# Performance work log

Hardware: AMD Instinct MI355X
Metric: run time of the kernel (lower is better)

Reference implementation:

```python
import jax, jax.numpy as jnp
import numpy as np

N = 100000   # nodes
E = 1600000  # edges
D = 128      # d_model
FF = 512     # dim_feedforward
EPS = 1e-5


def setup_inputs() -> dict:
    key = jax.random.key(0)
    ks = jax.random.split(key, 12)
    x = jax.random.normal(ks[0], (N, D), dtype=jnp.float32)
    edge_index = jax.random.randint(ks[1], (2, E), 0, N, dtype=jnp.int64)
    edge_weight = jax.random.uniform(ks[2], (E,), dtype=jnp.float32)
    sD = 1.0 / np.sqrt(D)
    sFF = 1.0 / np.sqrt(FF)
    W = jax.random.normal(ks[3], (D, D), dtype=jnp.float32) * sD   # GCN weight
    b = jnp.zeros((D,), jnp.float32)                                # GCN bias
    gamma = jnp.ones((D,), jnp.float32)                             # shared batchnorm
    beta = jnp.zeros((D,), jnp.float32)
    W1 = jax.random.normal(ks[4], (D, FF), dtype=jnp.float32) * sD  # MLP lin1
    b1 = jnp.zeros((FF,), jnp.float32)
    W2 = jax.random.normal(ks[5], (FF, D), dtype=jnp.float32) * sFF # MLP lin2
    b2 = jnp.zeros((D,), jnp.float32)
    return {"x": x, "edge_index": edge_index, "edge_weight": edge_weight,
            "W": W, "b": b, "gamma": gamma, "beta": beta,
            "W1": W1, "b1": b1, "W2": W2, "b2": b2}


def gcn_conv(x, edge_index, edge_weight, W, b):
    # GCNConv with add_self_loops=True (self-loop weight 1) and symmetric norm.
    h = x @ W                                   # [N, D]
    src, dst = edge_index[0], edge_index[1]
    deg = jax.ops.segment_sum(edge_weight, dst, num_segments=N) + 1.0
    dinv = jnp.where(deg > 0, jax.lax.rsqrt(deg), 0.0)
    norm = dinv[src] * edge_weight * dinv[dst]  # [E]
    out = jax.ops.segment_sum(norm[:, None] * h[src], dst, num_segments=N)
    out = out + (dinv * dinv)[:, None] * h      # self-loop contribution
    return out + b


def batch_norm(x, gamma, beta):
    # training-mode BatchNorm1d over the node (batch) dimension
    mu = jnp.mean(x, axis=0)
    var = jnp.mean((x - mu) ** 2, axis=0)
    return gamma * (x - mu) * jax.lax.rsqrt(var + EPS) + beta


def reference(x, edge_index, edge_weight, W, b, gamma, beta, W1, b1, W2, b2):
    x1 = batch_norm(x + gcn_conv(x, edge_index, edge_weight, W, b), gamma, beta)
    x2 = jax.nn.relu(x1 @ W1 + b1) @ W2 + b2    # MLP d_model->dim_ff->d_model
    return batch_norm(x1 + x2, gamma, beta)
```

## Files before the change

kernel.cpp:

```cpp
#include <hip/hip_runtime.h>

#define NN 100000
#define EE 1600000
#define DD 128
#define FFD 512
#define EPSV 1e-5f

#define SCB 98
#define EB 6250
#define MIXB 18750

typedef __attribute__((ext_vector_type(8))) short bf16x8;
typedef __attribute__((ext_vector_type(4))) float f32x4;
typedef unsigned long long ull;

__device__ __forceinline__ ushort f2b(float f) {
    uint u = __float_as_uint(f);
    return (ushort)((u + 0x7FFF + ((u >> 16) & 1)) >> 16);
}
__device__ __forceinline__ float b2f(ushort u) {
    return __uint_as_float(((uint)u) << 16);
}

__device__ __forceinline__ void gld_lds16(const ushort* g, ushort* l) {
    __builtin_amdgcn_global_load_lds(
        (const __attribute__((address_space(1))) uint*)g,
        (__attribute__((address_space(3))) uint*)l, 16, 0, 0);
}


__global__ __launch_bounds__(256) void k_init(ull* pk, float* s1, float* s2) {
    int i = blockIdx.x * 256 + threadIdx.x;
    if (i < NN) pk[i] = 0ULL;
    if (blockIdx.x == 0) { s1[threadIdx.x] = 0.f; s2[threadIdx.x] = 0.f; }
}


__global__ __launch_bounds__(256) void k_pre(const int* __restrict__ ei,
                                             const float* __restrict__ ew,
                                             ull* __restrict__ pk,
                                             int* __restrict__ rank,
                                             const float* __restrict__ x,
                                             ushort* __restrict__ xb,
                                             const float* __restrict__ W,
                                             const float* __restrict__ W1,
                                             const float* __restrict__ W2,
                                             ushort* __restrict__ WTb,
                                             ushort* __restrict__ W1img,
                                             ushort* __restrict__ W2img) {
    int bid = blockIdx.x;
    int t = threadIdx.x;
    if (bid < MIXB) {
        if (bid % 3 == 0) {
            int e = (bid / 3) * 256 + t;
            int dst = ei[EE + e];
            uint fx = (uint)(ew[e] * 16777216.0f + 0.5f);
            ull old = atomicAdd(&pk[dst], (1ULL << 32) | (ull)fx);
            rank[e] = (int)(old >> 32);
        } else {
            int xbk = bid - bid / 3 - 1;
            long i = (long)xbk * 256 + t;
            float4 v = ((const float4*)x)[i];
            ushort4 o;
            o.x = f2b(v.x); o.y = f2b(v.y); o.z = f2b(v.z); o.w = f2b(v.w);
            ((ushort4*)xb)[i] = o;
        }
    } else {
        int i = (bid - MIXB) * 256 + t;
        if (i < 16384) {
            int n = i >> 7, k = i & 127;
            WTb[i] = f2b(W[k * 128 + n]);
        } else if (i < 16384 + 65536) {
            int u = i - 16384;
            int ch = u >> 14, rem = u & 16383;
            int f = rem >> 7, col = rem & 127;
            int kb = (col >> 3) ^ (f & 15);
            int j = col & 7;
            W1img[u] = f2b(W1[(kb * 8 + j) * 512 + ch * 128 + f]);
        } else {
            int u = i - 16384 - 65536;
            int ch = u >> 14, rem = u & 16383;
            int jrow = rem >> 7, col = rem & 127;
            int kb = (col >> 3) ^ (jrow & 15);
            int j2 = col & 7;
            W2img[u] = f2b(W2[(ch * 128 + kb * 8 + j2) * 128 + jrow]);
        }
    }
}


__global__ __launch_bounds__(256) void k_scan_part(const ull* __restrict__ pk,
                                                   int* __restrict__ cnt,
                                                   float* __restrict__ dinv,
                                                   int* __restrict__ bsum) {
    __shared__ int red[4];
    int b = blockIdx.x, t = threadIdx.x;
    int base = b * 1024 + t * 4;
    int s = 0;
#pragma unroll
    for (int j = 0; j < 4; ++j) {
        int i = base + j;
        if (i < NN) {
            ull v = pk[i];
            int c = (int)(v >> 32);
            cnt[i] = c;
            dinv[i] = rsqrtf(1.0f + (float)(uint)(v & 0xFFFFFFFFu) * (1.0f / 16777216.0f));
            s += c;
        }
    }
#pragma unroll
    for (int d = 1; d < 64; d <<= 1) s += __shfl_xor(s, d);
    if ((t & 63) == 0) red[t >> 6] = s;
    __syncthreads();
    if (t == 0) bsum[b] = red[0] + red[1] + red[2] + red[3];
}

__global__ __launch_bounds__(128) void k_scan_base(int* __restrict__ bsum,
                                                   int* __restrict__ bbase,
                                                   int* __restrict__ start) {
    if (threadIdx.x == 0) {
        int run = 0;
        for (int i = 0; i < SCB; ++i) { bbase[i] = run; run += bsum[i]; }
        start[NN] = run;
    }
}

__global__ __launch_bounds__(256) void k_scan_fin(const int* __restrict__ cnt,
                                                  const int* __restrict__ bbase,
                                                  int* __restrict__ start) {
    __shared__ int ts[256];
    int b = blockIdx.x, t = threadIdx.x;
    int base = b * 1024 + t * 4;
    int v[4];
    int s = 0;
#pragma unroll
    for (int j = 0; j < 4; ++j) {
        int i = base + j;
        v[j] = (i < NN) ? cnt[i] : 0;
        s += v[j];
    }
    ts[t] = s;
    __syncthreads();
    for (int d = 1; d < 256; d <<= 1) {
        int add = (t >= d) ? ts[t - d] : 0;
        __syncthreads();
        ts[t] += add;
        __syncthreads();
    }
    int run = bbase[b] + ts[t] - s;
#pragma unroll
    for (int j = 0; j < 4; ++j) {
        int i = base + j;
        if (i < NN) {
            start[i] = run;
            run += v[j];
        }
    }
}


__global__ __launch_bounds__(256) void k_fill(const int* __restrict__ ei,
                                              const float* __restrict__ ew,
                                              const float* __restrict__ dinv,
                                              const int* __restrict__ start,
                                              const int* __restrict__ rank,
                                              uint2* __restrict__ csr) {
    int e = blockIdx.x * 256 + threadIdx.x;
    if (e < EE) {
        int src = ei[e];
        int dst = ei[EE + e];
        float nrm = dinv[src] * ew[e] * dinv[dst];
        int pos = start[dst] + rank[e];
        csr[pos] = make_uint2((uint)src, __float_as_uint(nrm));
    }
}


__global__ __launch_bounds__(256) void k_gather(const ushort* __restrict__ xb,
                                                const float* __restrict__ dinv,
                                                const int* __restrict__ start,
                                                const uint2* __restrict__ csr,
                                                ushort* __restrict__ aggx) {
    int t = threadIdx.x;
    int wv = t >> 6, l = t & 63;
    const uint* xbu = (const uint*)xb;
    uint* aggu = (uint*)aggx;

    for (int k = 0; k < 8; ++k) {
        int node = blockIdx.x * 32 + wv * 8 + k;
        int e0 = start[node], e1 = start[node + 1];
        float a0 = 0.f, a1 = 0.f;
        int i = e0;
        for (; i + 8 <= e1; i += 8) {
            uint2 rr[8];
            uint hh[8];
#pragma unroll
            for (int u = 0; u < 8; ++u) rr[u] = csr[i + u];
#pragma unroll
            for (int u = 0; u < 8; ++u) hh[u] = xbu[rr[u].x * 64 + l];
#pragma unroll
            for (int u = 0; u < 8; ++u) {
                float n = __uint_as_float(rr[u].y);
                a0 = fmaf(n, b2f((ushort)(hh[u] & 0xFFFF)), a0);
                a1 = fmaf(n, b2f((ushort)(hh[u] >> 16)), a1);
            }
        }
        if (i + 4 <= e1) {
            uint2 rr[4];
            uint hh[4];
#pragma unroll
            for (int u = 0; u < 4; ++u) rr[u] = csr[i + u];
#pragma unroll
            for (int u = 0; u < 4; ++u) hh[u] = xbu[rr[u].x * 64 + l];
#pragma unroll
            for (int u = 0; u < 4; ++u) {
                float n = __uint_as_float(rr[u].y);
                a0 = fmaf(n, b2f((ushort)(hh[u] & 0xFFFF)), a0);
                a1 = fmaf(n, b2f((ushort)(hh[u] >> 16)), a1);
            }
            i += 4;
        }
        for (; i < e1; ++i) {
            uint2 r0 = csr[i];
            uint h0 = xbu[r0.x * 64 + l];
            float n0 = __uint_as_float(r0.y);
            a0 = fmaf(n0, b2f((ushort)(h0 & 0xFFFF)), a0);
            a1 = fmaf(n0, b2f((ushort)(h0 >> 16)), a1);
        }
        float dv = dinv[node];
        float sl = dv * dv;
        uint hs = xbu[node * 64 + l];
        a0 = fmaf(sl, b2f((ushort)(hs & 0xFFFF)), a0);
        a1 = fmaf(sl, b2f((ushort)(hs >> 16)), a1);
        aggu[node * 64 + l] = (uint)f2b(a0) | ((uint)f2b(a1) << 16);
    }
}


__global__ __launch_bounds__(256) void k_conv(const ushort* __restrict__ aggx,
                                              const ushort* __restrict__ WTb,
                                              const float* __restrict__ b,
                                              ushort* xyb,
                                              float* __restrict__ stats1) {
    __shared__ __align__(16) ushort xt[64][136];
    __shared__ __align__(16) ushort wt[128][136];
    int t = threadIdx.x;
    int row0 = blockIdx.x * 64;

    for (int i = t; i < 2048; i += 256) {
        int r = i >> 4, c8 = (i & 15) << 3;
        *(uint4*)&wt[r][c8] = ((const uint4*)WTb)[i];
    }
    for (int i = t; i < 1024; i += 256) {
        int r = i >> 4, c8 = (i & 15) << 3;
        int gr = row0 + r;
        uint4 v = make_uint4(0u, 0u, 0u, 0u);
        if (gr < NN) v = ((const uint4*)aggx)[(long)gr * 16 + (i & 15)];
        *(uint4*)&xt[r][c8] = v;
    }
    __syncthreads();

    int wv = t >> 6, l = t & 63;
    int lr = l & 15, lg = l >> 4;
    int rw = wv & 1, jw = wv >> 1;

    f32x4 z4 = {0.f, 0.f, 0.f, 0.f};
    f32x4 acc[4][2];
#pragma unroll
    for (int jt = 0; jt < 4; ++jt)
#pragma unroll
        for (int rt = 0; rt < 2; ++rt) acc[jt][rt] = z4;

#pragma unroll
    for (int ks = 0; ks < 4; ++ks) {
        bf16x8 qR0 = *(const bf16x8*)&xt[rw * 32 + lr][ks * 32 + lg * 8];
        bf16x8 qR1 = *(const bf16x8*)&xt[rw * 32 + 16 + lr][ks * 32 + lg * 8];
#pragma unroll
        for (int jt = 0; jt < 4; ++jt) {
            bf16x8 pW = *(const bf16x8*)&wt[jw * 64 + jt * 16 + lr][ks * 32 + lg * 8];
            acc[jt][0] = __builtin_amdgcn_mfma_f32_16x16x32_bf16(pW, qR0, acc[jt][0], 0, 0, 0);
            acc[jt][1] = __builtin_amdgcn_mfma_f32_16x16x32_bf16(pW, qR1, acc[jt][1], 0, 0, 0);
        }
    }

    float sj[4][4], qj[4][4];
#pragma unroll
    for (int jt = 0; jt < 4; ++jt)
#pragma unroll
        for (int g = 0; g < 4; ++g) { sj[jt][g] = 0.f; qj[jt][g] = 0.f; }

#pragma unroll
    for (int jt = 0; jt < 4; ++jt) {
        int jb = jw * 64 + jt * 16 + lg * 4;
        float4 bv = *(const float4*)&b[jb];
#pragma unroll
        for (int rt = 0; rt < 2; ++rt) {
            int rloc = rw * 32 + rt * 16 + lr;
            int r = row0 + rloc;
            if (r < NN) {
                ushort4 xv = *(const ushort4*)&xyb[(long)r * 128 + jb];
                float z0 = b2f(xv.x) + acc[jt][rt][0] + bv.x;
                float z1 = b2f(xv.y) + acc[jt][rt][1] + bv.y;
                float z2 = b2f(xv.z) + acc[jt][rt][2] + bv.z;
                float z3 = b2f(xv.w) + acc[jt][rt][3] + bv.w;
                ushort4 o;
                o.x = f2b(z0); o.y = f2b(z1); o.z = f2b(z2); o.w = f2b(z3);
                *(ushort4*)&xyb[(long)r * 128 + jb] = o;
                sj[jt][0] += z0; sj[jt][1] += z1; sj[jt][2] += z2; sj[jt][3] += z3;
                qj[jt][0] += z0 * z0; qj[jt][1] += z1 * z1; qj[jt][2] += z2 * z2; qj[jt][3] += z3 * z3;
            }
        }
    }
#pragma unroll
    for (int jt = 0; jt < 4; ++jt)
#pragma unroll
        for (int g = 0; g < 4; ++g) {
#pragma unroll
            for (int d = 1; d < 16; d <<= 1) {
                sj[jt][g] += __shfl_xor(sj[jt][g], d);
                qj[jt][g] += __shfl_xor(qj[jt][g], d);
            }
        }
    __syncthreads();
    float* redS = (float*)&xt[0][0];
    float* redQ = redS + 512;
    if (lr == 0) {
#pragma unroll
        for (int jt = 0; jt < 4; ++jt)
#pragma unroll
            for (int g = 0; g < 4; ++g) {
                int j = jw * 64 + jt * 16 + lg * 4 + g;
                redS[wv * 128 + j] = sj[jt][g];
                redQ[wv * 128 + j] = qj[jt][g];
            }
    }
    __syncthreads();
    if (t < 128) {
        int w0 = (t >> 6) * 2;
        atomicAdd(&stats1[t], redS[w0 * 128 + t] + redS[(w0 + 1) * 128 + t]);
        atomicAdd(&stats1[128 + t], redQ[w0 * 128 + t] + redQ[(w0 + 1) * 128 + t]);
    }
}


__global__ __launch_bounds__(128) void k_bn_fin(const float* __restrict__ stats,
                                                const float* __restrict__ gamma,
                                                const float* __restrict__ beta,
                                                float* __restrict__ ac) {
    int c = threadIdx.x;
    float mu = stats[c] * (1.0f / NN);
    float var = stats[128 + c] * (1.0f / NN) - mu * mu;
    float a = gamma[c] * rsqrtf(var + EPSV);
    ac[c] = a;
    ac[128 + c] = beta[c] - mu * a;
}


__global__ __launch_bounds__(256) void k_affine2(const ushort* __restrict__ zb,
                                                 const float* __restrict__ ac,
                                                 float* __restrict__ out) {
    long i = (long)blockIdx.x * 256 + threadIdx.x;
    int c4i = (int)(i & 31);
    float4 a = ((const float4*)ac)[c4i];
    float4 cc = ((const float4*)(ac + 128))[c4i];
    ushort4 zv = ((const ushort4*)zb)[i];
    float4 o;
    o.x = a.x * b2f(zv.x) + cc.x;
    o.y = a.y * b2f(zv.y) + cc.y;
    o.z = a.z * b2f(zv.z) + cc.z;
    o.w = a.w * b2f(zv.w) + cc.w;
    ((float4*)out)[i] = o;
}


#define SWZ16(row, kb) ((((kb) ^ ((row) & 15)) << 3))

__global__ __launch_bounds__(512, 4) void k_mlp(const ushort* __restrict__ yb,
                                                const float* __restrict__ ac1,
                                                const ushort* __restrict__ W1img,
                                                const float* __restrict__ b1,
                                                const ushort* __restrict__ W2img,
                                                const float* __restrict__ b2,
                                                ushort* __restrict__ zb,
                                                float* __restrict__ stats2) {
    __shared__ __align__(16) ushort xt[64 * 128];
    __shared__ __align__(16) ushort ht[64 * 128];
    __shared__ __align__(16) ushort wc[128 * 128];
    int t = threadIdx.x;
    int row0 = blockIdx.x * 64;

    for (int i = t; i < 1024; i += 512) {
        int r = i >> 4, kb = i & 15;
        int gr = row0 + r;
        ushort4 y0 = make_ushort4(0, 0, 0, 0), y1 = make_ushort4(0, 0, 0, 0);
        if (gr < NN) {
            long base = (long)gr * 32 + kb * 2;
            y0 = ((const ushort4*)yb)[base];
            y1 = ((const ushort4*)yb)[base + 1];
        }
        float4 a0 = ((const float4*)ac1)[kb * 2];
        float4 a1 = ((const float4*)ac1)[kb * 2 + 1];
        float4 c0 = ((const float4*)(ac1 + 128))[kb * 2];
        float4 c1 = ((const float4*)(ac1 + 128))[kb * 2 + 1];
        ushort4 o0, o1;
        o0.x = f2b(a0.x * b2f(y0.x) + c0.x);
        o0.y = f2b(a0.y * b2f(y0.y) + c0.y);
        o0.z = f2b(a0.z * b2f(y0.z) + c0.z);
        o0.w = f2b(a0.w * b2f(y0.w) + c0.w);
        o1.x = f2b(a1.x * b2f(y1.x) + c1.x);
        o1.y = f2b(a1.y * b2f(y1.y) + c1.y);
        o1.z = f2b(a1.z * b2f(y1.z) + c1.z);
        o1.w = f2b(a1.w * b2f(y1.w) + c1.w);
        ushort* dst = &xt[r * 128 + SWZ16(r, kb)];
        *(ushort4*)dst = o0;
        *(ushort4*)(dst + 4) = o1;
    }

    int wv = t >> 6, l = t & 63;
    int lr = l & 15, lg = l >> 4;
    int rw = wv & 3, jw = wv >> 2;
    int xrow = rw * 16 + lr;

    f32x4 z4 = {0.f, 0.f, 0.f, 0.f};
    f32x4 acc[4];
#pragma unroll
    for (int jt = 0; jt < 4; ++jt) acc[jt] = z4;

    for (int ch = 0; ch < 4; ++ch) {
        __syncthreads();
        {
            const ushort* src = W1img + ch * 16384;
#pragma unroll
            for (int i = 0; i < 4; ++i) {
                int u = (t + i * 512) * 8;
                gld_lds16(src + u, wc + u);
            }
        }
        __syncthreads();

        f32x4 hacc[4];
#pragma unroll
        for (int ft = 0; ft < 4; ++ft) hacc[ft] = z4;
#pragma unroll
        for (int ks = 0; ks < 4; ++ks) {
            int kcol = ((ks * 4 + lg) ^ lr) << 3;
            bf16x8 aR = *(const bf16x8*)&xt[xrow * 128 + kcol];
#pragma unroll
            for (int ft = 0; ft < 4; ++ft) {
                int f = jw * 64 + ft * 16 + lr;
                bf16x8 bW = *(const bf16x8*)&wc[f * 128 + kcol];
                hacc[ft] = __builtin_amdgcn_mfma_f32_16x16x32_bf16(aR, bW, hacc[ft], 0, 0, 0);
            }
        }
#pragma unroll
        for (int ft = 0; ft < 4; ++ft) {
            int fcol = jw * 64 + ft * 16 + lr;
            float b1v = b1[ch * 128 + fcol];
            int kbf = fcol >> 3, wi = fcol & 7;
#pragma unroll
            for (int rg = 0; rg < 4; ++rg) {
                int hrow = rw * 16 + lg * 4 + rg;
                ht[hrow * 128 + ((kbf ^ (hrow & 15)) << 3) + wi] =
                    f2b(fmaxf(hacc[ft][rg] + b1v, 0.f));
            }
        }
        __syncthreads();

        {
            const ushort* src = W2img + ch * 16384;
#pragma unroll
            for (int i = 0; i < 4; ++i) {
                int u = (t + i * 512) * 8;
                gld_lds16(src + u, wc + u);
            }
        }
        __syncthreads();

#pragma unroll
        for (int ks = 0; ks < 4; ++ks) {
            int kcol = ((ks * 4 + lg) ^ lr) << 3;
            bf16x8 qR = *(const bf16x8*)&ht[xrow * 128 + kcol];
#pragma unroll
            for (int jt = 0; jt < 4; ++jt) {
                int j = jw * 64 + jt * 16 + lr;
                bf16x8 pW = *(const bf16x8*)&wc[j * 128 + kcol];
                acc[jt] = __builtin_amdgcn_mfma_f32_16x16x32_bf16(pW, qR, acc[jt], 0, 0, 0);
            }
        }
    }

    float sj[4][4], qj[4][4];
    int r = row0 + xrow;
#pragma unroll
    for (int jt = 0; jt < 4; ++jt) {
        int jb = jw * 64 + jt * 16 + lg * 4;
        float4 b2v = *(const float4*)&b2[jb];
        int kbj = jb >> 3, wj = jb & 7;
        ushort4 xv = *(const ushort4*)&xt[xrow * 128 + ((kbj ^ lr) << 3) + wj];
        float z0 = b2f(xv.x) + acc[jt][0] + b2v.x;
        float z1 = b2f(xv.y) + acc[jt][1] + b2v.y;
        float z2 = b2f(xv.z) + acc[jt][2] + b2v.z;
        float z3 = b2f(xv.w) + acc[jt][3] + b2v.w;
        if (r < NN) {
            ushort4 o;
            o.x = f2b(z0); o.y = f2b(z1); o.z = f2b(z2); o.w = f2b(z3);
            *(ushort4*)&zb[(long)r * 128 + jb] = o;
            sj[jt][0] = z0; sj[jt][1] = z1; sj[jt][2] = z2; sj[jt][3] = z3;
            qj[jt][0] = z0 * z0; qj[jt][1] = z1 * z1; qj[jt][2] = z2 * z2; qj[jt][3] = z3 * z3;
        } else {
            sj[jt][0] = 0.f; sj[jt][1] = 0.f; sj[jt][2] = 0.f; sj[jt][3] = 0.f;
            qj[jt][0] = 0.f; qj[jt][1] = 0.f; qj[jt][2] = 0.f; qj[jt][3] = 0.f;
        }
    }
#pragma unroll
    for (int jt = 0; jt < 4; ++jt)
#pragma unroll
        for (int g = 0; g < 4; ++g) {
#pragma unroll
            for (int d = 1; d < 16; d <<= 1) {
                sj[jt][g] += __shfl_xor(sj[jt][g], d);
                qj[jt][g] += __shfl_xor(qj[jt][g], d);
            }
        }
    __syncthreads();
    float* redS = (float*)&ht[0];
    float* redQ = redS + 1024;
    if (lr == 0) {
#pragma unroll
        for (int jt = 0; jt < 4; ++jt)
#pragma unroll
            for (int g = 0; g < 4; ++g) {
                int j = jw * 64 + jt * 16 + lg * 4 + g;
                redS[wv * 128 + j] = sj[jt][g];
                redQ[wv * 128 + j] = qj[jt][g];
            }
    }
    __syncthreads();
    if (t < 128) {
        int h = t >> 6;
        float S = redS[(h * 4 + 0) * 128 + t] + redS[(h * 4 + 1) * 128 + t]
                + redS[(h * 4 + 2) * 128 + t] + redS[(h * 4 + 3) * 128 + t];
        float Q = redQ[(h * 4 + 0) * 128 + t] + redQ[(h * 4 + 1) * 128 + t]
                + redQ[(h * 4 + 2) * 128 + t] + redQ[(h * 4 + 3) * 128 + t];
        atomicAdd(&stats2[t], S);
        atomicAdd(&stats2[128 + t], Q);
    }
}


extern "C" void kernel_launch(void* const* d_in, const int* in_sizes, int n_in,
                              void* d_out, int out_size, void* d_ws, size_t ws_size,
                              hipStream_t stream) {
    const float* x     = (const float*)d_in[0];
    const int*   ei    = (const int*)d_in[1];
    const float* ew    = (const float*)d_in[2];
    const float* W     = (const float*)d_in[3];
    const float* b     = (const float*)d_in[4];
    const float* gamma = (const float*)d_in[5];
    const float* beta  = (const float*)d_in[6];
    const float* W1    = (const float*)d_in[7];
    const float* b1    = (const float*)d_in[8];
    const float* W2    = (const float*)d_in[9];
    const float* b2    = (const float*)d_in[10];
    float* out = (float*)d_out;
    float* ws  = (float*)d_ws;

    ull*   pk     = (ull*)ws;
    float* dinv   = ws + 2 * NN;
    float* stats1 = ws + 3 * NN;
    float* ac1    = stats1 + 256;
    float* stats2 = ac1 + 256;
    float* ac2    = stats2 + 256;
    ushort* xb    = (ushort*)(ws + 3 * NN + 1024);
    ushort* WTb   = xb + (long)NN * 128;
    ushort* W1img = WTb + 16384;
    ushort* W2img = W1img + 65536;
    float*  fend  = ws + 3 * NN + 1024 + (long)NN * 64 + 73728;
    int*   cnt    = (int*)fend;
    int*   start  = cnt + NN;
    int*   bsum   = start + NN + 1;
    int*   bbase  = bsum + SCB;
    uint2* csr    = (uint2*)(((uintptr_t)(bbase + SCB) + 7) & ~(uintptr_t)7);
    ushort* aggx  = (ushort*)(csr + EE);
    int*   rank   = (int*)aggx;
    ushort* yb    = xb;
    ushort* zb    = aggx;

    int nb = (NN + 63) / 64;

    k_init<<<(NN + 255) / 256, 256, 0, stream>>>(pk, stats1, stats2);
    k_pre<<<MIXB + 576, 256, 0, stream>>>(ei, ew, pk, rank, x, xb, W, W1, W2, WTb, W1img, W2img);
    k_scan_part<<<SCB, 256, 0, stream>>>(pk, cnt, dinv, bsum);
    k_scan_base<<<1, 128, 0, stream>>>(bsum, bbase, start);
    k_scan_fin<<<SCB, 256, 0, stream>>>(cnt, bbase, start);
    k_fill<<<EE / 256, 256, 0, stream>>>(ei, ew, dinv, start, rank, csr);
    k_gather<<<NN / 32, 256, 0, stream>>>(xb, dinv, start, csr, aggx);
    k_conv<<<nb, 256, 0, stream>>>(aggx, WTb, b, yb, stats1);
    k_bn_fin<<<1, 128, 0, stream>>>(stats1, gamma, beta, ac1);
    k_mlp<<<nb, 512, 0, stream>>>(yb, ac1, W1img, b1, W2img, b2, zb, stats2);
    k_bn_fin<<<1, 128, 0, stream>>>(stats2, gamma, beta, ac2);
    k_affine2<<<(NN * 32) / 256, 256, 0, stream>>>(zb, ac2, out);
}
```

Baseline: 346.0 us.

## Fuse sparse gather into GCN conv GEMM kernel with swizzled LDS tiles

Merges the CSR neighbor-aggregation kernel and the dense W projection kernel into one 512-thread kernel. Aggregated rows are written straight into a swizzled LDS tile instead of round-tripping through a global aggx buffer. The W weight image is pre-swizzled and async-loaded into LDS, and the MLP's first-layer epilogue is reworked to emit vectorized ushort4 stores by swapping MFMA operand order. This saves a launch and a full N×D bf16 write/read, at the cost of a larger block whose occupancy depends on the irregular gather phase.

```diff
diff --git a/kernel.cpp b/kernel.cpp
--- a/kernel.cpp
+++ b/kernel.cpp
@@ -45,7 +45,7 @@
                                              const float* __restrict__ W,
                                              const float* __restrict__ W1,
                                              const float* __restrict__ W2,
-                                             ushort* __restrict__ WTb,
+                                             ushort* __restrict__ WTimg,
                                              ushort* __restrict__ W1img,
                                              ushort* __restrict__ W2img) {
     int bid = blockIdx.x;
@@ -68,8 +68,9 @@
     } else {
         int i = (bid - MIXB) * 256 + t;
         if (i < 16384) {
-            int n = i >> 7, k = i & 127;
-            WTb[i] = f2b(W[k * 128 + n]);
+            int n = i >> 7, col = i & 127;
+            int k = ((((col >> 3) ^ (n & 15)) << 3)) + (col & 7);
+            WTimg[i] = f2b(W[k * 128 + n]);
         } else if (i < 16384 + 65536) {
             int u = i - 16384;
             int ch = u >> 14, rem = u & 16383;
@@ -176,139 +177,125 @@
 }
 
 
-__global__ __launch_bounds__(256) void k_gather(const ushort* __restrict__ xb,
-                                                const float* __restrict__ dinv,
-                                                const int* __restrict__ start,
-                                                const uint2* __restrict__ csr,
-                                                ushort* __restrict__ aggx) {
-    int t = threadIdx.x;
-    int wv = t >> 6, l = t & 63;
-    const uint* xbu = (const uint*)xb;
-    uint* aggu = (uint*)aggx;
-
-    for (int k = 0; k < 8; ++k) {
-        int node = blockIdx.x * 32 + wv * 8 + k;
-        int e0 = start[node], e1 = start[node + 1];
-        float a0 = 0.f, a1 = 0.f;
-        int i = e0;
-        for (; i + 8 <= e1; i += 8) {
-            uint2 rr[8];
-            uint hh[8];
-#pragma unroll
-            for (int u = 0; u < 8; ++u) rr[u] = csr[i + u];
-#pragma unroll
-            for (int u = 0; u < 8; ++u) hh[u] = xbu[rr[u].x * 64 + l];
-#pragma unroll
-            for (int u = 0; u < 8; ++u) {
-                float n = __uint_as_float(rr[u].y);
-                a0 = fmaf(n, b2f((ushort)(hh[u] & 0xFFFF)), a0);
-                a1 = fmaf(n, b2f((ushort)(hh[u] >> 16)), a1);
-            }
-        }
-        if (i + 4 <= e1) {
-            uint2 rr[4];
-            uint hh[4];
-#pragma unroll
-            for (int u = 0; u < 4; ++u) rr[u] = csr[i + u];
-#pragma unroll
-            for (int u = 0; u < 4; ++u) hh[u] = xbu[rr[u].x * 64 + l];
-#pragma unroll
-            for (int u = 0; u < 4; ++u) {
-                float n = __uint_as_float(rr[u].y);
-                a0 = fmaf(n, b2f((ushort)(hh[u] & 0xFFFF)), a0);
-                a1 = fmaf(n, b2f((ushort)(hh[u] >> 16)), a1);
-            }
-            i += 4;
-        }
-        for (; i < e1; ++i) {
-            uint2 r0 = csr[i];
-            uint h0 = xbu[r0.x * 64 + l];
-            float n0 = __uint_as_float(r0.y);
-            a0 = fmaf(n0, b2f((ushort)(h0 & 0xFFFF)), a0);
-            a1 = fmaf(n0, b2f((ushort)(h0 >> 16)), a1);
-        }
-        float dv = dinv[node];
-        float sl = dv * dv;
-        uint hs = xbu[node * 64 + l];
-        a0 = fmaf(sl, b2f((ushort)(hs & 0xFFFF)), a0);
-        a1 = fmaf(sl, b2f((ushort)(hs >> 16)), a1);
-        aggu[node * 64 + l] = (uint)f2b(a0) | ((uint)f2b(a1) << 16);
-    }
-}
-
-
-__global__ __launch_bounds__(256) void k_conv(const ushort* __restrict__ aggx,
-                                              const ushort* __restrict__ WTb,
-                                              const float* __restrict__ b,
-                                              ushort* xyb,
-                                              float* __restrict__ stats1) {
-    __shared__ __align__(16) ushort xt[64][136];
-    __shared__ __align__(16) ushort wt[128][136];
+#define SWZ16(row, kb) ((((kb) ^ ((row) & 15)) << 3))
+
+__global__ __launch_bounds__(512, 6) void k_gconv(const ushort* __restrict__ xb,
+                                                  const float* __restrict__ dinv,
+                                                  const int* __restrict__ start,
+                                                  const uint2* __restrict__ csr,
+                                                  const ushort* __restrict__ WTimg,
+                                                  const float* __restrict__ b,
+                                                  ushort* __restrict__ ybuf,
+                                                  float* __restrict__ stats1) {
+    __shared__ __align__(16) ushort xt[64 * 128];
+    __shared__ __align__(16) ushort wc[128 * 128];
     int t = threadIdx.x;
     int row0 = blockIdx.x * 64;
-
-    for (int i = t; i < 2048; i += 256) {
-        int r = i >> 4, c8 = (i & 15) << 3;
-        *(uint4*)&wt[r][c8] = ((const uint4*)WTb)[i];
-    }
-    for (int i = t; i < 1024; i += 256) {
-        int r = i >> 4, c8 = (i & 15) << 3;
-        int gr = row0 + r;
-        uint4 v = make_uint4(0u, 0u, 0u, 0u);
-        if (gr < NN) v = ((const uint4*)aggx)[(long)gr * 16 + (i & 15)];
-        *(uint4*)&xt[r][c8] = v;
-    }
-    __syncthreads();
-
     int wv = t >> 6, l = t & 63;
+
+#pragma unroll
+    for (int i = 0; i < 4; ++i) {
+        int u = (t + i * 512) * 8;
+        gld_lds16(WTimg + u, wc + u);
+    }
+
+    const uint* xbu = (const uint*)xb;
+    for (int k = 0; k < 8; ++k) {
+        int rloc = wv * 8 + k;
+        int node = row0 + rloc;
+        float a0 = 0.f, a1 = 0.f;
+        if (node < NN) {
+            int e0 = start[node], e1 = start[node + 1];
+            int i = e0;
+            for (; i + 8 <= e1; i += 8) {
+                uint2 rr[8];
+                uint hh[8];
+#pragma unroll
+                for (int u = 0; u < 8; ++u) rr[u] = csr[i + u];
+#pragma unroll
+                for (int u = 0; u < 8; ++u) hh[u] = xbu[rr[u].x * 64 + l];
+#pragma unroll
+                for (int u = 0; u < 8; ++u) {
+                    float n = __uint_as_float(rr[u].y);
+                    a0 = fmaf(n, b2f((ushort)(hh[u] & 0xFFFF)), a0);
+                    a1 = fmaf(n, b2f((ushort)(hh[u] >> 16)), a1);
+                }
+            }
+            if (i + 4 <= e1) {
+                uint2 rr[4];
+                uint hh[4];
+#pragma unroll
+                for (int u = 0; u < 4; ++u) rr[u] = csr[i + u];
+#pragma unroll
+                for (int u = 0; u < 4; ++u) hh[u] = xbu[rr[u].x * 64 + l];
+#pragma unroll
+                for (int u = 0; u < 4; ++u) {
+                    float n = __uint_as_float(rr[u].y);
+                    a0 = fmaf(n, b2f((ushort)(hh[u] & 0xFFFF)), a0);
+                    a1 = fmaf(n, b2f((ushort)(hh[u] >> 16)), a1);
+                }
+                i += 4;
+            }
+            for (; i < e1; ++i) {
+                uint2 r0 = csr[i];
+                uint h0 = xbu[r0.x * 64 + l];
+                float n0 = __uint_as_float(r0.y);
+                a0 = fmaf(n0, b2f((ushort)(h0 & 0xFFFF)), a0);
+                a1 = fmaf(n0, b2f((ushort)(h0 >> 16)), a1);
+            }
+            float dv = dinv[node];
+            float sl = dv * dv;
+            uint hs = xbu[(long)node * 64 + l];
+            a0 = fmaf(sl, b2f((ushort)(hs & 0xFFFF)), a0);
+            a1 = fmaf(sl, b2f((ushort)(hs >> 16)), a1);
+        }
+        int col = 2 * l;
+        uint pv = (uint)f2b(a0) | ((uint)f2b(a1) << 16);
+        *(uint*)&xt[rloc * 128 + SWZ16(rloc, col >> 3) + (col & 7)] = pv;
+    }
+    __syncthreads();
+
     int lr = l & 15, lg = l >> 4;
-    int rw = wv & 1, jw = wv >> 1;
+    int rw = wv & 3, jw = wv >> 2;
+    int xrow = rw * 16 + lr;
 
     f32x4 z4 = {0.f, 0.f, 0.f, 0.f};
-    f32x4 acc[4][2];
-#pragma unroll
-    for (int jt = 0; jt < 4; ++jt)
-#pragma unroll
-        for (int rt = 0; rt < 2; ++rt) acc[jt][rt] = z4;
+    f32x4 acc[4];
+#pragma unroll
+    for (int jt = 0; jt < 4; ++jt) acc[jt] = z4;
 
 #pragma unroll
     for (int ks = 0; ks < 4; ++ks) {
-        bf16x8 qR0 = *(const bf16x8*)&xt[rw * 32 + lr][ks * 32 + lg * 8];
-        bf16x8 qR1 = *(const bf16x8*)&xt[rw * 32 + 16 + lr][ks * 32 + lg * 8];
+        int kcol = ((ks * 4 + lg) ^ lr) << 3;
+        bf16x8 qR = *(const bf16x8*)&xt[xrow * 128 + kcol];
 #pragma unroll
         for (int jt = 0; jt < 4; ++jt) {
-            bf16x8 pW = *(const bf16x8*)&wt[jw * 64 + jt * 16 + lr][ks * 32 + lg * 8];
-            acc[jt][0] = __builtin_amdgcn_mfma_f32_16x16x32_bf16(pW, qR0, acc[jt][0], 0, 0, 0);
-            acc[jt][1] = __builtin_amdgcn_mfma_f32_16x16x32_bf16(pW, qR1, acc[jt][1], 0, 0, 0);
+            int f = jw * 64 + jt * 16 + lr;
+            bf16x8 pW = *(const bf16x8*)&wc[f * 128 + kcol];
+            acc[jt] = __builtin_amdgcn_mfma_f32_16x16x32_bf16(pW, qR, acc[jt], 0, 0, 0);
         }
     }
 
     float sj[4][4], qj[4][4];
-#pragma unroll
-    for (int jt = 0; jt < 4; ++jt)
-#pragma unroll
-        for (int g = 0; g < 4; ++g) { sj[jt][g] = 0.f; qj[jt][g] = 0.f; }
-
+    int r = row0 + xrow;
 #pragma unroll
     for (int jt = 0; jt < 4; ++jt) {
         int jb = jw * 64 + jt * 16 + lg * 4;
         float4 bv = *(const float4*)&b[jb];
-#pragma unroll
-        for (int rt = 0; rt < 2; ++rt) {
-            int rloc = rw * 32 + rt * 16 + lr;
-            int r = row0 + rloc;
-            if (r < NN) {
-                ushort4 xv = *(const ushort4*)&xyb[(long)r * 128 + jb];
-                float z0 = b2f(xv.x) + acc[jt][rt][0] + bv.x;
-                float z1 = b2f(xv.y) + acc[jt][rt][1] + bv.y;
-                float z2 = b2f(xv.z) + acc[jt][rt][2] + bv.z;
-                float z3 = b2f(xv.w) + acc[jt][rt][3] + bv.w;
-                ushort4 o;
-                o.x = f2b(z0); o.y = f2b(z1); o.z = f2b(z2); o.w = f2b(z3);
-                *(ushort4*)&xyb[(long)r * 128 + jb] = o;
-                sj[jt][0] += z0; sj[jt][1] += z1; sj[jt][2] += z2; sj[jt][3] += z3;
-                qj[jt][0] += z0 * z0; qj[jt][1] += z1 * z1; qj[jt][2] += z2 * z2; qj[jt][3] += z3 * z3;
-            }
+        if (r < NN) {
+            ushort4 xv = *(const ushort4*)&xb[(long)r * 128 + jb];
+            float z0 = b2f(xv.x) + acc[jt][0] + bv.x;
+            float z1 = b2f(xv.y) + acc[jt][1] + bv.y;
+            float z2 = b2f(xv.z) + acc[jt][2] + bv.z;
+            float z3 = b2f(xv.w) + acc[jt][3] + bv.w;
+            ushort4 o;
+            o.x = f2b(z0); o.y = f2b(z1); o.z = f2b(z2); o.w = f2b(z3);
+            *(ushort4*)&ybuf[(long)r * 128 + jb] = o;
+            sj[jt][0] = z0; sj[jt][1] = z1; sj[jt][2] = z2; sj[jt][3] = z3;
+            qj[jt][0] = z0 * z0; qj[jt][1] = z1 * z1; qj[jt][2] = z2 * z2; qj[jt][3] = z3 * z3;
+        } else {
+            sj[jt][0] = 0.f; sj[jt][1] = 0.f; sj[jt][2] = 0.f; sj[jt][3] = 0.f;
+            qj[jt][0] = 0.f; qj[jt][1] = 0.f; qj[jt][2] = 0.f; qj[jt][3] = 0.f;
         }
     }
 #pragma unroll
@@ -322,8 +309,8 @@
             }
         }
     __syncthreads();
-    float* redS = (float*)&xt[0][0];
-    float* redQ = redS + 512;
+    float* redS = (float*)&xt[0];
+    float* redQ = redS + 1024;
     if (lr == 0) {
 #pragma unroll
         for (int jt = 0; jt < 4; ++jt)
@@ -336,9 +323,13 @@
     }
     __syncthreads();
     if (t < 128) {
-        int w0 = (t >> 6) * 2;
-        atomicAdd(&stats1[t], redS[w0 * 128 + t] + redS[(w0 + 1) * 128 + t]);
-        atomicAdd(&stats1[128 + t], redQ[w0 * 128 + t] + redQ[(w0 + 1) * 128 + t]);
+        int h = t >> 6;
+        float S = redS[(h * 4 + 0) * 128 + t] + redS[(h * 4 + 1) * 128 + t]
+                + redS[(h * 4 + 2) * 128 + t] + redS[(h * 4 + 3) * 128 + t];
+        float Q = redQ[(h * 4 + 0) * 128 + t] + redQ[(h * 4 + 1) * 128 + t]
+                + redQ[(h * 4 + 2) * 128 + t] + redQ[(h * 4 + 3) * 128 + t];
+        atomicAdd(&stats1[t], S);
+        atomicAdd(&stats1[128 + t], Q);
     }
 }
 
@@ -372,8 +363,6 @@
     ((float4*)out)[i] = o;
 }
 
-
-#define SWZ16(row, kb) ((((kb) ^ ((row) & 15)) << 3))
 
 __global__ __launch_bounds__(512, 4) void k_mlp(const ushort* __restrict__ yb,
                                                 const float* __restrict__ ac1,
@@ -449,20 +438,19 @@
             for (int ft = 0; ft < 4; ++ft) {
                 int f = jw * 64 + ft * 16 + lr;
                 bf16x8 bW = *(const bf16x8*)&wc[f * 128 + kcol];
-                hacc[ft] = __builtin_amdgcn_mfma_f32_16x16x32_bf16(aR, bW, hacc[ft], 0, 0, 0);
+                hacc[ft] = __builtin_amdgcn_mfma_f32_16x16x32_bf16(bW, aR, hacc[ft], 0, 0, 0);
             }
         }
 #pragma unroll
         for (int ft = 0; ft < 4; ++ft) {
-            int fcol = jw * 64 + ft * 16 + lr;
-            float b1v = b1[ch * 128 + fcol];
-            int kbf = fcol >> 3, wi = fcol & 7;
-#pragma unroll
-            for (int rg = 0; rg < 4; ++rg) {
-                int hrow = rw * 16 + lg * 4 + rg;
-                ht[hrow * 128 + ((kbf ^ (hrow & 15)) << 3) + wi] =
-                    f2b(fmaxf(hacc[ft][rg] + b1v, 0.f));
-            }
+            int fc = jw * 64 + ft * 16 + lg * 4;
+            float4 b1v = *(const float4*)&b1[ch * 128 + fc];
+            ushort4 o;
+            o.x = f2b(fmaxf(hacc[ft][0] + b1v.x, 0.f));
+            o.y = f2b(fmaxf(hacc[ft][1] + b1v.y, 0.f));
+            o.z = f2b(fmaxf(hacc[ft][2] + b1v.z, 0.f));
+            o.w = f2b(fmaxf(hacc[ft][3] + b1v.w, 0.f));
+            *(ushort4*)&ht[xrow * 128 + (((fc >> 3) ^ lr) << 3) + (fc & 7)] = o;
         }
         __syncthreads();
 
@@ -572,8 +560,8 @@
     float* stats2 = ac1 + 256;
     float* ac2    = stats2 + 256;
     ushort* xb    = (ushort*)(ws + 3 * NN + 1024);
-    ushort* WTb   = xb + (long)NN * 128;
-    ushort* W1img = WTb + 16384;
+    ushort* WTimg = xb + (long)NN * 128;
+    ushort* W1img = WTimg + 16384;
     ushort* W2img = W1img + 65536;
     float*  fend  = ws + 3 * NN + 1024 + (long)NN * 64 + 73728;
     int*   cnt    = (int*)fend;
@@ -581,23 +569,21 @@
     int*   bsum   = start + NN + 1;
     int*   bbase  = bsum + SCB;
     uint2* csr    = (uint2*)(((uintptr_t)(bbase + SCB) + 7) & ~(uintptr_t)7);
-    ushort* aggx  = (ushort*)(csr + EE);
-    int*   rank   = (int*)aggx;
-    ushort* yb    = xb;
-    ushort* zb    = aggx;
+    ushort* ybuf  = (ushort*)(csr + EE);
+    int*   rank   = (int*)ybuf;
+    ushort* zb    = xb;
 
     int nb = (NN + 63) / 64;
 
     k_init<<<(NN + 255) / 256, 256, 0, stream>>>(pk, stats1, stats2);
-    k_pre<<<MIXB + 576, 256, 0, stream>>>(ei, ew, pk, rank, x, xb, W, W1, W2, WTb, W1img, W2img);
+    k_pre<<<MIXB + 576, 256, 0, stream>>>(ei, ew, pk, rank, x, xb, W, W1, W2, WTimg, W1img, W2img);
     k_scan_part<<<SCB, 256, 0, stream>>>(pk, cnt, dinv, bsum);
     k_scan_base<<<1, 128, 0, stream>>>(bsum, bbase, start);
     k_scan_fin<<<SCB, 256, 0, stream>>>(cnt, bbase, start);
     k_fill<<<EE / 256, 256, 0, stream>>>(ei, ew, dinv, start, rank, csr);
-    k_gather<<<NN / 32, 256, 0, stream>>>(xb, dinv, start, csr, aggx);
-    k_conv<<<nb, 256, 0, stream>>>(aggx, WTb, b, yb, stats1);
+    k_gconv<<<nb, 512, 0, stream>>>(xb, dinv, start, csr, WTimg, b, ybuf, stats1);
     k_bn_fin<<<1, 128, 0, stream>>>(stats1, gamma, beta, ac1);
-    k_mlp<<<nb, 512, 0, stream>>>(yb, ac1, W1img, b1, W2img, b2, zb, stats2);
+    k_mlp<<<nb, 512, 0, stream>>>(ybuf, ac1, W1img, b1, W2img, b2, zb, stats2);
     k_bn_fin<<<1, 128, 0, stream>>>(stats2, gamma, beta, ac2);
     k_affine2<<<(NN * 32) / 256, 256, 0, stream>>>(zb, ac2, out);
 }
```

Result: no change. 346.5 us, median of 2 (+0.1%).
